# Optimization experiments

Measured on AMD Instinct MI355X. Metric: run time of the kernel, lower is better.

Reference implementation:

```python
import jax, jax.numpy as jnp
import numpy as np

B, D, C = 512, 16384, 3
SAMPLE_DURATION = 16
NEG_THRESHOLD = 0.5
NEGPOS_RATIO = 3


def setup_inputs() -> dict:
    key = jax.random.key(0)
    k1, k2, k3, k4, k5, k6, k7 = jax.random.split(key, 7)
    loc_pred = jax.random.normal(k1, (B, D, 2), dtype=jnp.float32)
    conf_pred = jax.random.normal(k2, (B, D, C), dtype=jnp.float32)
    # one ground-truth (start, end, label) per sample, within [0, 16]
    start = jax.random.uniform(k3, (B,), dtype=jnp.float32) * 8.0
    length = 1.0 + jax.random.uniform(k4, (B,), dtype=jnp.float32) * 7.0
    label = jax.random.randint(k5, (B,), 0, C).astype(jnp.float32)
    targets = jnp.stack([start, start + length, label], axis=-1)  # [B,3]
    # default bars stored as (center, length) in frame units
    centers = 1.0 + jax.random.uniform(k6, (D,), dtype=jnp.float32) * (SAMPLE_DURATION - 2.0)
    lengths = 1.0 + jax.random.uniform(k7, (D,), dtype=jnp.float32) * (SAMPLE_DURATION - 4.0)
    default_bar = jnp.stack([centers, lengths], axis=-1)  # [D,2]
    return {"loc_pred": loc_pred, "conf_pred": conf_pred,
            "targets": targets, "default_bar": default_bar}


def _match_one(truth, label, default):
    """truth [2]=(start,end), label scalar int, default [D,2]=(center,length).
    Returns loc_t [D,2], conf_t [D] (0=ignore, 1=background, >1=fg)."""
    d_c, d_l = default[:, 0], default[:, 1]
    d_s, d_e = d_c - d_l * 0.5, d_c + d_l * 0.5
    inter = jnp.clip(jnp.minimum(truth[1], d_e) - jnp.maximum(truth[0], d_s), 0.0)
    union = (truth[1] - truth[0]) + (d_e - d_s) - inter
    ov = inter / union                                   # [D] 1-D IoU
    best_prior = jnp.argmax(ov)                          # best anchor for the truth
    bto = ov.at[best_prior].set(2.0)                     # index_fill_ with 2
    conf = jnp.full((D,), label + 1, dtype=jnp.int32)    # single truth -> broadcast
    is_bg = conf == 1
    conf = jnp.where(bto < NEG_THRESHOLD, 0, conf)
    conf = jnp.where(is_bg, 1, conf)
    # SSD-style encoding of matched (start,end) against (center,length)
    m_c = (truth[0] + truth[1]) * 0.5
    m_l = truth[1] - truth[0]
    loc = jnp.stack([(m_c - d_c) / d_l, jnp.log(m_l / d_l)], axis=-1)  # [D,2]
    return loc, conf


def reference(loc_pred, conf_pred, targets, default_bar):
    truths = targets[:, :2]                              # [B,2]
    labels = targets[:, 2].astype(jnp.int32)             # [B]
    loc_t, conf_t = jax.vmap(_match_one, in_axes=(0, 0, None))(truths, labels, default_bar)
    loc_t = jax.lax.stop_gradient(loc_t)                 # built under no_grad in torch
    conf_t = jax.lax.stop_gradient(conf_t)

    pos = conf_t > 0                                     # [B,D] used for mining
    loc_pos = conf_t > 1                                 # [B,D] used for loc loss

    # SmoothL1 (beta=1), reduction='sum' over positives
    diff = loc_pred - loc_t
    ad = jnp.abs(diff)
    sl1 = jnp.where(ad < 1.0, 0.5 * diff * diff, ad - 0.5)
    loss_loc = jnp.sum(sl1 * loc_pos[..., None].astype(sl1.dtype))

    # hard-negative mining on per-anchor CE surrogate
    conf_tc = jnp.clip(conf_t - 1, 0)                    # [B,D] class ids 0..C-1
    lse = jax.nn.logsumexp(conf_pred, axis=-1)           # [B,D]
    gathered = jnp.take_along_axis(conf_pred, conf_tc[..., None], axis=-1)[..., 0]
    lc = lse - gathered
    lc = jnp.where(pos, 0.0, lc)
    loss_idx = jnp.argsort(-lc, axis=1)                  # descending sort
    idx_rank = jnp.argsort(loss_idx, axis=1)
    num_pos = jnp.sum(pos.astype(jnp.int32), axis=1, keepdims=True)   # [B,1]
    num_neg = jnp.clip(NEGPOS_RATIO * num_pos, max=D - 1)
    neg = idx_rank < num_neg                             # [B,D]

    sel = (pos | neg).astype(conf_pred.dtype)
    logp = jax.nn.log_softmax(conf_pred, axis=-1)
    ce = -jnp.take_along_axis(logp, conf_tc[..., None], axis=-1)[..., 0]
    loss_conf = jnp.sum(ce * sel)

    N = jnp.sum(num_pos).astype(loss_loc.dtype)
    return jnp.stack([loss_loc / N, loss_conf / N])
```

## Files before the change

kernel.cpp:

```cpp
#include <hip/hip_runtime.h>
#include <hip/hip_fp16.h>
#include <math.h>

constexpr int Bn = 512;
constexpr int Dn = 16384;
constexpr int BS = 512;
constexpr int CHUNKS = 16;
constexpr int CPRI = Dn / CHUNKS;
constexpr int K1T = 512;

__device__ __forceinline__ float lse3(float a, float b, float c) {
  float m = fmaxf(a, fmaxf(b, c));
  return m + __logf(__expf(a - m) + __expf(b - m) + __expf(c - m));
}
__device__ __forceinline__ float sl1f(float x) {
  float a = fabsf(x);
  return a < 1.f ? 0.5f * x * x : a - 0.5f;
}

__device__ __forceinline__ double blockReduceAddD(double v, double* sred) {
  int t = threadIdx.x;
  sred[t] = v;
  __syncthreads();
  for (int off = BS >> 1; off > 0; off >>= 1) {
    if (t < off) sred[t] += sred[t + off];
    __syncthreads();
  }
  double r = sred[0];
  __syncthreads();
  return r;
}

__global__ __launch_bounds__(K1T) void multiloss_stream(
    const float* __restrict__ loc_pred, const float* __restrict__ conf_pred,
    const float* __restrict__ targets, const float* __restrict__ default_bar,
    unsigned short* __restrict__ lc16,
    float* __restrict__ pce, float* __restrict__ plloc, int* __restrict__ pnpos)
{
  __shared__ float s_conf[CPRI * 3];
  __shared__ float s_bar[CPRI * 2];
  __shared__ unsigned short s_plist[CPRI];
  __shared__ float s_red[24];

  const int bid = blockIdx.x;
  const int b = bid >> 4, c = bid & 15;
  const int t = threadIdx.x;
  const int l = t & 63, w = t >> 6;
  const int wb = t & ~63;

  {
    const float4* srcC = (const float4*)(conf_pred + (size_t)b * Dn * 3) + (size_t)c * 768;
    float4* dstC = (float4*)s_conf;
    __builtin_amdgcn_global_load_lds(
        (const __attribute__((address_space(1))) void*)(srcC + t),
        (__attribute__((address_space(3))) void*)(dstC + wb), 16, 0, 0);
    if (t < 256)
      __builtin_amdgcn_global_load_lds(
          (const __attribute__((address_space(1))) void*)(srcC + 512 + t),
          (__attribute__((address_space(3))) void*)(dstC + 512 + wb), 16, 0, 0);
    const float4* srcB = (const float4*)default_bar + (size_t)c * 512;
    float4* dstB = (float4*)s_bar;
    __builtin_amdgcn_global_load_lds(
        (const __attribute__((address_space(1))) void*)(srcB + t),
        (__attribute__((address_space(3))) void*)(dstB + wb), 16, 0, 0);
  }

  const float t0  = targets[b * 3 + 0];
  const float t1  = targets[b * 3 + 1];
  const int   lab = (int)targets[b * 3 + 2];

  float ce = 0.f, lloc = 0.f; int npos = 0;
  const float m_c = (t0 + t1) * 0.5f;
  const float m_l = t1 - t0;
  const float T   = t1 - t0;

  __syncthreads();

  if (lab == 0) {
    #pragma unroll
    for (int i = 0; i < CPRI / K1T; ++i) {
      int p = i * K1T + t;
      float c0 = s_conf[3 * p], c1 = s_conf[3 * p + 1], c2 = s_conf[3 * p + 2];
      float hi = fmaxf(c0, c1), lo = fminf(c0, c1);
      float m  = fmaxf(hi, c2), mid = fminf(hi, c2);
      float s  = 1.f + __expf(lo - m) + __expf(mid - m);
      ce += (m - c0) + __logf(s);
    }
  } else {
    unsigned short* __restrict__ lcrow = lc16 + (size_t)b * Dn + (size_t)c * CPRI;
    unsigned wcnt = 0;
    unsigned short* plist = s_plist + (w << 7);
    #pragma unroll
    for (int i = 0; i < 2; ++i) {
      const int p = (w << 7) + (i << 6) + l;
      float c0 = s_conf[3 * p], c1 = s_conf[3 * p + 1], c2 = s_conf[3 * p + 2];
      float2 db = ((const float2*)s_bar)[p];
      float d_c = db.x, d_l = db.y;
      float d_s = __fmaf_rn(-0.5f, d_l, d_c);
      float d_e = __fmaf_rn(0.5f, d_l, d_c);
      float inter = fmaxf(fminf(t1, d_e) - fmaxf(t0, d_s), 0.f);
      float uni = (T + d_l) - inter;
      bool pos = (2.f * inter >= uni);
      npos += pos;
      float hi = fmaxf(c0, c1), lo = fminf(c0, c1);
      float m  = fmaxf(hi, c2), mid = fminf(hi, c2);
      float s  = 1.f + __expf(lo - m) + __expf(mid - m);
      float lnS = __logf(s);
      float cl = (lab == 1) ? c1 : c2;
      ce += pos ? ((m - cl) + lnS) : 0.f;
      float lcv = pos ? 0.f : ((m - c0) + lnS);
      lcrow[p] = __half_as_ushort(__float2half(lcv));
      unsigned long long mask = __ballot(pos);
      if (pos) {
        unsigned off = __builtin_amdgcn_mbcnt_hi((unsigned)(mask >> 32),
                       __builtin_amdgcn_mbcnt_lo((unsigned)mask, 0u));
        plist[wcnt + off] = (unsigned short)p;
      }
      wcnt += (unsigned)__popcll(mask);
    }
    const float log_ml = __logf(m_l);
    const float2* __restrict__ lp2 = (const float2*)loc_pred + (size_t)b * Dn + (size_t)c * CPRI;
    for (unsigned j = l; j < wcnt; j += 64) {
      int p = plist[j];
      float2 db = ((const float2*)s_bar)[p];
      float2 lp = lp2[p];
      float pd0 = lp.x - __fdividef(m_c - db.x, db.y);
      float pd1 = (lp.y - log_ml) + __logf(db.y);
      lloc += sl1f(pd0) + sl1f(pd1);
    }
  }

  #pragma unroll
  for (int off = 1; off < 64; off <<= 1) {
    ce   += __shfl_xor(ce, off);
    lloc += __shfl_xor(lloc, off);
    npos += __shfl_xor(npos, off);
  }
  if (l == 0) {
    s_red[w * 3 + 0] = ce; s_red[w * 3 + 1] = lloc; s_red[w * 3 + 2] = __int_as_float(npos);
  }
  __syncthreads();
  if (t == 0) {
    float Ce = 0.f, Ll = 0.f; int Np = 0;
    #pragma unroll
    for (int k = 0; k < 8; ++k) {
      Ce += s_red[k * 3 + 0]; Ll += s_red[k * 3 + 1]; Np += __float_as_int(s_red[k * 3 + 2]);
    }
    int pidx = b * CHUNKS + c;
    pce[pidx] = Ce; plloc[pidx] = Ll; pnpos[pidx] = Np;
  }
}

__global__ __launch_bounds__(BS) void multiloss_select(
    const float* __restrict__ loc_pred, const float* __restrict__ conf_pred,
    const float* __restrict__ targets, const float* __restrict__ default_bar,
    const unsigned short* __restrict__ lc16,
    const float* __restrict__ pce, const float* __restrict__ plloc,
    const int* __restrict__ pnpos,
    double* __restrict__ rloc, double* __restrict__ rconf, double* __restrict__ rnp)
{
  __shared__ unsigned short s_lc[Dn];
  __shared__ int      s_hist[256];
  __shared__ double   s_dred[BS];
  __shared__ float    s_fv[BS];
  __shared__ int      s_fi[BS];
  __shared__ unsigned s_wt[8];
  __shared__ unsigned s_sel[2];
  __shared__ double   s_sc[2];
  __shared__ int      s_np;

  const int b = blockIdx.x;
  const int t = threadIdx.x;
  const int lab = (int)targets[b * 3 + 2];

  if (lab == 0) {
    if (t == 0) {
      double ce = 0.0;
      for (int kk = 0; kk < CHUNKS; ++kk) ce += (double)pce[CHUNKS * b + kk];
      rloc[b] = 0.0; rconf[b] = ce; rnp[b] = (double)Dn;
    }
    return;
  }

  const float t0 = targets[b * 3 + 0];
  const float t1 = targets[b * 3 + 1];

  const float4* lcr = (const float4*)(lc16 + (size_t)b * Dn);
  float4* sl4 = (float4*)s_lc;
  #pragma unroll
  for (int j = 0; j < Dn / 8 / BS; ++j) sl4[j * BS + t] = lcr[j * BS + t];
  __syncthreads();

  if (t == 0) {
    double ce = 0.0, ll = 0.0; int np = 0;
    for (int kk = 0; kk < CHUNKS; ++kk) {
      int pi = CHUNKS * b + kk;
      ce += (double)pce[pi]; ll += (double)plloc[pi]; np += pnpos[pi];
    }
    s_sc[0] = ce; s_sc[1] = ll; s_np = np;
  }
  __syncthreads();
  int np = s_np;

  if (np == 0) {
    float bV = -1.f; int bI = 0;
    for (int d = t; d < Dn; d += BS) {
      float2 db = ((const float2*)default_bar)[d];
      float d_s = db.x - db.y * 0.5f;
      float d_e = db.x + db.y * 0.5f;
      float inter = fmaxf(fminf(t1, d_e) - fmaxf(t0, d_s), 0.f);
      float uni = (t1 - t0) + (d_e - d_s) - inter;
      float ov = inter / uni;
      if (ov > bV) { bV = ov; bI = d; }
    }
    s_fv[t] = bV; s_fi[t] = bI;
    __syncthreads();
    for (int off = BS >> 1; off > 0; off >>= 1) {
      if (t < off) {
        float v2 = s_fv[t + off]; int i2 = s_fi[t + off];
        if (v2 > s_fv[t] || (v2 == s_fv[t] && i2 < s_fi[t])) { s_fv[t] = v2; s_fi[t] = i2; }
      }
      __syncthreads();
    }
    if (t == 0) {
      int d = s_fi[0];
      const float* cp = conf_pred + (size_t)b * Dn * 3 + (size_t)d * 3;
      float c0 = cp[0], c1 = cp[1], c2 = cp[2];
      float lse = lse3(c0, c1, c2);
      float cl = (lab == 1) ? c1 : c2;
      float2 db = ((const float2*)default_bar)[d];
      float2 lp = ((const float2*)loc_pred)[(size_t)b * Dn + d];
      float m_c = (t0 + t1) * 0.5f, m_l = t1 - t0;
      float pd0 = lp.x - (m_c - db.x) / db.y;
      float pd1 = lp.y - __logf(m_l / db.y);
      s_sc[0] += (double)(lse - cl);
      s_sc[1] += (double)(sl1f(pd0) + sl1f(pd1));
      s_np = 1;
      s_lc[d] = 0;
    }
    __syncthreads();
    np = s_np;
  }
  const int k = min(3 * np, Dn - 1);

  unsigned prefix = 0;
  int K = k;
  const int lane = t & 63, w = t >> 6;
  for (int r = 0; r < 2; ++r) {
    if (t < 256) s_hist[t] = 0;
    __syncthreads();
    for (int d = t; d < Dn; d += BS) {
      unsigned u = s_lc[d];
      bool ok = (r == 0) || ((u >> 8) == prefix);
      if (ok) {
        unsigned bin = (r == 0) ? (u >> 8) : (u & 0xFFu);
        atomicAdd(&s_hist[bin], 1);
      }
    }
    __syncthreads();
    unsigned psum = (t < 256) ? (unsigned)s_hist[t] : 0u;
    unsigned incl = psum;
    #pragma unroll
    for (int off = 1; off < 64; off <<= 1) {
      unsigned v = __shfl_down(incl, off, 64);
      if (lane + off < 64) incl += v;
    }
    if (lane == 0) s_wt[w] = incl;
    __syncthreads();
    unsigned aboveW = 0;
    for (int w2 = w + 1; w2 < 8; ++w2) aboveW += s_wt[w2];
    const unsigned above = aboveW + (incl - psum);
    if (t < 256 && above < (unsigned)K && (unsigned)K <= above + psum) {
      s_sel[0] = (unsigned)t;
      s_sel[1] = above;
    }
    __syncthreads();
    unsigned selBin = s_sel[0];
    K -= (int)s_sel[1];
    prefix = (r == 0) ? selBin : ((prefix << 8) | selBin);
    __syncthreads();
  }
  const unsigned tb = prefix;

  float    ssum = 0.f;
  unsigned scnt = 0;
  for (int d = t; d < Dn; d += BS) {
    unsigned u = s_lc[d];
    if (u > tb) {
      ssum += __half2float(__ushort_as_half((unsigned short)u));
      scnt++;
    }
  }
  double S = blockReduceAddD((double)ssum, s_dred);
  double C = blockReduceAddD((double)scnt, s_dred);

  if (t == 0) {
    double tval = (double)__half2float(__ushort_as_half((unsigned short)tb));
    double topk = S + ((double)k - C) * tval;
    rloc[b]  = s_sc[1];
    rconf[b] = s_sc[0] + topk;
    rnp[b]   = (double)np;
  }
}

__global__ __launch_bounds__(BS) void multiloss_mono(
    const float* __restrict__ loc_pred, const float* __restrict__ conf_pred,
    const float* __restrict__ targets, const float* __restrict__ default_bar,
    double* __restrict__ rloc, double* __restrict__ rconf, double* __restrict__ rnp)
{
  __shared__ float    s_lc[Dn];
  __shared__ int      s_hist[2048];
  __shared__ unsigned s_scan[BS];
  __shared__ double   s_dred[BS];
  __shared__ unsigned s_sel[2];
  __shared__ double   s_corr[2];
  __shared__ int      s_np;

  const int b = blockIdx.x;
  const int t = threadIdx.x;

  const float t0  = targets[b * 3 + 0];
  const float t1  = targets[b * 3 + 1];
  const int   lab = (int)targets[b * 3 + 2];

  const float* __restrict__ cpb = conf_pred + (size_t)b * Dn * 3;

  if (lab == 0) {
    float ce = 0.f;
    for (int d = t; d < Dn; d += BS) {
      const float* cp = cpb + d * 3;
      ce += lse3(cp[0], cp[1], cp[2]) - cp[0];
    }
    double tot = blockReduceAddD((double)ce, s_dred);
    if (t == 0) { rloc[b] = 0.0; rconf[b] = tot; rnp[b] = (double)Dn; }
    return;
  }

  const float m_c = (t0 + t1) * 0.5f;
  const float m_l = t1 - t0;

  float bestV = -1.f; int bestI = 0;
  int   nposL = 0;
  float cePosL = 0.f;
  float llocL  = 0.f;

  for (int d = t; d < Dn; d += BS) {
    float2 db = ((const float2*)default_bar)[d];
    float d_c = db.x, d_l = db.y;
    float d_s = d_c - d_l * 0.5f;
    float d_e = d_c + d_l * 0.5f;
    float inter = fmaxf(fminf(t1, d_e) - fmaxf(t0, d_s), 0.f);
    float uni = (t1 - t0) + (d_e - d_s) - inter;
    float ov  = inter / uni;

    const float* cp = cpb + d * 3;
    float c0 = cp[0];
    float lse = lse3(cp[0], cp[1], cp[2]);

    if (ov > bestV) { bestV = ov; bestI = d; }

    float lcv;
    if (ov >= 0.5f) {
      nposL++;
      float cl = (lab == 1) ? cp[1] : cp[2];
      cePosL += lse - cl;
      float2 lp = ((const float2*)loc_pred)[(size_t)b * Dn + d];
      float pd0 = lp.x - (m_c - d_c) / d_l;
      float pd1 = lp.y - __logf(m_l / d_l);
      llocL += sl1f(pd0) + sl1f(pd1);
      lcv = 0.f;
    } else {
      lcv = lse - c0;
    }
    s_lc[d] = lcv;
  }

  float* sv = (float*)s_hist;
  int*   si = (int*)(s_hist + BS);
  sv[t] = bestV; si[t] = bestI;
  __syncthreads();
  for (int off = BS >> 1; off > 0; off >>= 1) {
    if (t < off) {
      float v2 = sv[t + off]; int i2 = si[t + off];
      if (v2 > sv[t] || (v2 == sv[t] && i2 < si[t])) { sv[t] = v2; si[t] = i2; }
    }
    __syncthreads();
  }
  float bV = sv[0]; int bI = si[0];
  __syncthreads();

  double nposTot  = blockReduceAddD((double)nposL, s_dred);
  double cePosTot = blockReduceAddD((double)cePosL, s_dred);
  double llocTot  = blockReduceAddD((double)llocL, s_dred);
  int num_pos = (int)(nposTot + 0.5);

  if (t == 0) {
    double cc = 0.0, lcor = 0.0; int np2 = num_pos;
    if (bV < 0.5f) {
      int d = bI;
      const float* cp = cpb + d * 3;
      float lse = lse3(cp[0], cp[1], cp[2]);
      float cl = (lab == 1) ? cp[1] : cp[2];
      cc = (double)(lse - cl);
      float2 db = ((const float2*)default_bar)[d];
      float2 lp = ((const float2*)loc_pred)[(size_t)b * Dn + d];
      float pd0 = lp.x - (m_c - db.x) / db.y;
      float pd1 = lp.y - __logf(m_l / db.y);
      lcor = (double)(sl1f(pd0) + sl1f(pd1));
      np2 += 1;
      s_lc[d] = 0.f;
    }
    s_corr[0] = cc; s_corr[1] = lcor; s_np = np2;
  }
  __syncthreads();
  int np = s_np;
  int k  = min(3 * np, Dn - 1);

  unsigned prefix = 0;
  int K = k;
  for (int r = 0; r < 3; ++r) {
    for (int i = t; i < 2048; i += BS) s_hist[i] = 0;
    __syncthreads();
    for (int d = t; d < Dn; d += BS) {
      unsigned u = __float_as_uint(s_lc[d]);
      bool ok = (r == 0) || (r == 1 ? ((u >> 21) == prefix) : ((u >> 10) == prefix));
      if (ok) {
        unsigned bin = (r == 0) ? (u >> 21)
                     : (r == 1) ? ((u >> 10) & 0x7FFu)
                                : (u & 0x3FFu);
        atomicAdd(&s_hist[bin], 1);
      }
    }
    __syncthreads();
    int nb  = (r == 2) ? 1024 : 2048;
    int per = nb / BS;
    unsigned psum = 0;
    for (int j = 0; j < per; ++j) psum += (unsigned)s_hist[t * per + j];
    s_scan[t] = psum;
    __syncthreads();
    for (int off = 1; off < BS; off <<= 1) {
      unsigned v = (t + off < BS) ? s_scan[t + off] : 0u;
      __syncthreads();
      s_scan[t] += v;
      __syncthreads();
    }
    unsigned above = (t < BS - 1) ? s_scan[t + 1] : 0u;
    if (above < (unsigned)K && (unsigned)K <= above + psum) {
      unsigned cum = above;
      int found = 0;
      for (int j = per - 1; j >= 0; --j) {
        unsigned c = (unsigned)s_hist[t * per + j];
        if (cum + c >= (unsigned)K) { found = j; break; }
        cum += c;
      }
      s_sel[0] = (unsigned)(t * per + found);
      s_sel[1] = cum;
    }
    __syncthreads();
    unsigned selBin = s_sel[0];
    K -= (int)s_sel[1];
    prefix = (r == 0) ? selBin
           : (r == 1) ? ((prefix << 11) | selBin)
                      : ((prefix << 10) | selBin);
    __syncthreads();
  }
  const unsigned tb = prefix;

  float    ssum = 0.f;
  unsigned scnt = 0;
  for (int d = t; d < Dn; d += BS) {
    float v = s_lc[d];
    if (__float_as_uint(v) > tb) { ssum += v; scnt++; }
  }
  double S = blockReduceAddD((double)ssum, s_dred);
  double C = blockReduceAddD((double)scnt, s_dred);

  if (t == 0) {
    double tval = (double)__uint_as_float(tb);
    double topk = S + ((double)k - C) * tval;
    rloc[b]  = llocTot + s_corr[1];
    rconf[b] = cePosTot + s_corr[0] + topk;
    rnp[b]   = (double)s_np;
  }
}

__global__ __launch_bounds__(512) void multiloss_final(
    const double* __restrict__ rloc, const double* __restrict__ rconf,
    const double* __restrict__ rnp, float* __restrict__ out)
{
  __shared__ double s1[512], s2[512], s3[512];
  int t = threadIdx.x;
  s1[t] = rloc[t];
  s2[t] = rconf[t];
  s3[t] = rnp[t];
  __syncthreads();
  for (int off = 256; off > 0; off >>= 1) {
    if (t < off) { s1[t] += s1[t + off]; s2[t] += s2[t + off]; s3[t] += s3[t + off]; }
    __syncthreads();
  }
  if (t == 0) {
    double N = s3[0];
    out[0] = (float)(s1[0] / N);
    out[1] = (float)(s2[0] / N);
  }
}

extern "C" void kernel_launch(void* const* d_in, const int* in_sizes, int n_in,
                              void* d_out, int out_size, void* d_ws, size_t ws_size,
                              hipStream_t stream) {
  const float* loc_pred    = (const float*)d_in[0];
  const float* conf_pred   = (const float*)d_in[1];
  const float* targets     = (const float*)d_in[2];
  const float* default_bar = (const float*)d_in[3];
  float* out = (float*)d_out;
  char* ws = (char*)d_ws;

  constexpr size_t LC_BYTES = (size_t)Bn * Dn * sizeof(unsigned short);
  constexpr size_t P_CNT = (size_t)Bn * CHUNKS;
  size_t off = LC_BYTES;
  float*  pce   = (float*)(ws + off); off += P_CNT * 4;
  float*  plloc = (float*)(ws + off); off += P_CNT * 4;
  int*    pnpos = (int*)(ws + off);   off += P_CNT * 4;
  double* rloc  = (double*)(ws + off); off += Bn * 8;
  double* rconf = (double*)(ws + off); off += Bn * 8;
  double* rnp   = (double*)(ws + off); off += Bn * 8;
  const size_t NEED = off;

  if (ws_size >= NEED) {
    hipLaunchKernelGGL(multiloss_stream, dim3(Bn * CHUNKS), dim3(K1T), 0, stream,
                       loc_pred, conf_pred, targets, default_bar,
                       (unsigned short*)ws, pce, plloc, pnpos);
    hipLaunchKernelGGL(multiloss_select, dim3(Bn), dim3(BS), 0, stream,
                       loc_pred, conf_pred, targets, default_bar,
                       (const unsigned short*)ws, pce, plloc, pnpos,
                       rloc, rconf, rnp);
    hipLaunchKernelGGL(multiloss_final, dim3(1), dim3(512), 0, stream,
                       rloc, rconf, rnp, out);
  } else {
    double* mloc  = (double*)ws;
    double* mconf = mloc + Bn;
    double* mnp   = mconf + Bn;
    hipLaunchKernelGGL(multiloss_mono, dim3(Bn), dim3(BS), 0, stream,
                       loc_pred, conf_pred, targets, default_bar, mloc, mconf, mnp);
    hipLaunchKernelGGL(multiloss_final, dim3(1), dim3(512), 0, stream,
                       mloc, mconf, mnp, out);
  }
}
```

Measured before the change: 62.05 us.

## Map two adjacent priors per thread with vector LDS reads and packed half2 stores

The streaming kernel now uses 32 chunks per batch row and 256-thread blocks. Each thread processes two adjacent priors, reading confidences and bars from LDS as float2/float4 vectors. It writes both surrogate losses as a single packed half2 word. The per-wave ballot/prefix compaction of positive priors is replaced by a direct predicated loc_pred load inside each lane. The aim is fewer LDS and global store instructions, no compaction overhead and more blocks in flight, at the cost of divergent, uncoalesced loc_pred loads for positives.

```diff
diff --git a/kernel.cpp b/kernel.cpp
--- a/kernel.cpp
+++ b/kernel.cpp
@@ -5,9 +5,9 @@
 constexpr int Bn = 512;
 constexpr int Dn = 16384;
 constexpr int BS = 512;
-constexpr int CHUNKS = 16;
+constexpr int CHUNKS = 32;
 constexpr int CPRI = Dn / CHUNKS;
-constexpr int K1T = 512;
+constexpr int K1T = 256;
 
 __device__ __forceinline__ float lse3(float a, float b, float c) {
   float m = fmaxf(a, fmaxf(b, c));
@@ -34,31 +34,30 @@
 __global__ __launch_bounds__(K1T) void multiloss_stream(
     const float* __restrict__ loc_pred, const float* __restrict__ conf_pred,
     const float* __restrict__ targets, const float* __restrict__ default_bar,
-    unsigned short* __restrict__ lc16,
+    unsigned* __restrict__ lc32,
     float* __restrict__ pce, float* __restrict__ plloc, int* __restrict__ pnpos)
 {
   __shared__ float s_conf[CPRI * 3];
   __shared__ float s_bar[CPRI * 2];
-  __shared__ unsigned short s_plist[CPRI];
-  __shared__ float s_red[24];
+  __shared__ float s_red[12];
 
   const int bid = blockIdx.x;
-  const int b = bid >> 4, c = bid & 15;
+  const int b = bid >> 5, c = bid & 31;
   const int t = threadIdx.x;
   const int l = t & 63, w = t >> 6;
   const int wb = t & ~63;
 
   {
-    const float4* srcC = (const float4*)(conf_pred + (size_t)b * Dn * 3) + (size_t)c * 768;
+    const float4* srcC = (const float4*)(conf_pred + (size_t)b * Dn * 3) + (size_t)c * (CPRI * 3 / 4);
     float4* dstC = (float4*)s_conf;
     __builtin_amdgcn_global_load_lds(
         (const __attribute__((address_space(1))) void*)(srcC + t),
         (__attribute__((address_space(3))) void*)(dstC + wb), 16, 0, 0);
-    if (t < 256)
+    if (t < 128)
       __builtin_amdgcn_global_load_lds(
-          (const __attribute__((address_space(1))) void*)(srcC + 512 + t),
-          (__attribute__((address_space(3))) void*)(dstC + 512 + wb), 16, 0, 0);
-    const float4* srcB = (const float4*)default_bar + (size_t)c * 512;
+          (const __attribute__((address_space(1))) void*)(srcC + 256 + t),
+          (__attribute__((address_space(3))) void*)(dstC + 256 + wb), 16, 0, 0);
+    const float4* srcB = (const float4*)default_bar + (size_t)c * (CPRI * 2 / 4);
     float4* dstB = (float4*)s_bar;
     __builtin_amdgcn_global_load_lds(
         (const __attribute__((address_space(1))) void*)(srcB + t),
@@ -71,63 +70,81 @@
 
   float ce = 0.f, lloc = 0.f; int npos = 0;
   const float m_c = (t0 + t1) * 0.5f;
-  const float m_l = t1 - t0;
   const float T   = t1 - t0;
 
   __syncthreads();
 
+  const float2 ca  = ((const float2*)s_conf)[3 * t];
+  const float2 cb  = ((const float2*)s_conf)[3 * t + 1];
+  const float2 cc_ = ((const float2*)s_conf)[3 * t + 2];
+
   if (lab == 0) {
-    #pragma unroll
-    for (int i = 0; i < CPRI / K1T; ++i) {
-      int p = i * K1T + t;
-      float c0 = s_conf[3 * p], c1 = s_conf[3 * p + 1], c2 = s_conf[3 * p + 2];
-      float hi = fmaxf(c0, c1), lo = fminf(c0, c1);
-      float m  = fmaxf(hi, c2), mid = fminf(hi, c2);
+    {
+      float hi = fmaxf(ca.x, ca.y), lo = fminf(ca.x, ca.y);
+      float m  = fmaxf(hi, cb.x),  mid = fminf(hi, cb.x);
       float s  = 1.f + __expf(lo - m) + __expf(mid - m);
-      ce += (m - c0) + __logf(s);
+      ce += (m - ca.x) + __logf(s);
+    }
+    {
+      float hi = fmaxf(cb.y, cc_.x), lo = fminf(cb.y, cc_.x);
+      float m  = fmaxf(hi, cc_.y),  mid = fminf(hi, cc_.y);
+      float s  = 1.f + __expf(lo - m) + __expf(mid - m);
+      ce += (m - cb.y) + __logf(s);
     }
   } else {
-    unsigned short* __restrict__ lcrow = lc16 + (size_t)b * Dn + (size_t)c * CPRI;
-    unsigned wcnt = 0;
-    unsigned short* plist = s_plist + (w << 7);
-    #pragma unroll
-    for (int i = 0; i < 2; ++i) {
-      const int p = (w << 7) + (i << 6) + l;
-      float c0 = s_conf[3 * p], c1 = s_conf[3 * p + 1], c2 = s_conf[3 * p + 2];
-      float2 db = ((const float2*)s_bar)[p];
-      float d_c = db.x, d_l = db.y;
-      float d_s = __fmaf_rn(-0.5f, d_l, d_c);
-      float d_e = __fmaf_rn(0.5f, d_l, d_c);
-      float inter = fmaxf(fminf(t1, d_e) - fmaxf(t0, d_s), 0.f);
-      float uni = (T + d_l) - inter;
+    const float log_ml = __logf(T);
+    const float2* __restrict__ lp2 = (const float2*)loc_pred + (size_t)b * Dn + (size_t)c * CPRI;
+    const float4 bb = ((const float4*)s_bar)[t];
+    float lcv0, lcv1;
+    const int pA = 2 * t;
+
+    {
+      float dc = bb.x, dl = bb.y;
+      float ds = __fmaf_rn(-0.5f, dl, dc);
+      float de = __fmaf_rn(0.5f, dl, dc);
+      float inter = fmaxf(fminf(t1, de) - fmaxf(t0, ds), 0.f);
+      float uni = (T + dl) - inter;
       bool pos = (2.f * inter >= uni);
-      npos += pos;
-      float hi = fmaxf(c0, c1), lo = fminf(c0, c1);
-      float m  = fmaxf(hi, c2), mid = fminf(hi, c2);
+      float hi = fmaxf(ca.x, ca.y), lo = fminf(ca.x, ca.y);
+      float m  = fmaxf(hi, cb.x),  mid = fminf(hi, cb.x);
       float s  = 1.f + __expf(lo - m) + __expf(mid - m);
       float lnS = __logf(s);
-      float cl = (lab == 1) ? c1 : c2;
+      float cl = (lab == 1) ? ca.y : cb.x;
+      npos += pos;
       ce += pos ? ((m - cl) + lnS) : 0.f;
-      float lcv = pos ? 0.f : ((m - c0) + lnS);
-      lcrow[p] = __half_as_ushort(__float2half(lcv));
-      unsigned long long mask = __ballot(pos);
+      lcv0 = pos ? 0.f : ((m - ca.x) + lnS);
       if (pos) {
-        unsigned off = __builtin_amdgcn_mbcnt_hi((unsigned)(mask >> 32),
-                       __builtin_amdgcn_mbcnt_lo((unsigned)mask, 0u));
-        plist[wcnt + off] = (unsigned short)p;
+        float2 lp = lp2[pA];
+        float pd0 = lp.x - __fdividef(m_c - dc, dl);
+        float pd1 = (lp.y - log_ml) + __logf(dl);
+        lloc += sl1f(pd0) + sl1f(pd1);
       }
-      wcnt += (unsigned)__popcll(mask);
-    }
-    const float log_ml = __logf(m_l);
-    const float2* __restrict__ lp2 = (const float2*)loc_pred + (size_t)b * Dn + (size_t)c * CPRI;
-    for (unsigned j = l; j < wcnt; j += 64) {
-      int p = plist[j];
-      float2 db = ((const float2*)s_bar)[p];
-      float2 lp = lp2[p];
-      float pd0 = lp.x - __fdividef(m_c - db.x, db.y);
-      float pd1 = (lp.y - log_ml) + __logf(db.y);
-      lloc += sl1f(pd0) + sl1f(pd1);
-    }
+    }
+    {
+      float dc = bb.z, dl = bb.w;
+      float ds = __fmaf_rn(-0.5f, dl, dc);
+      float de = __fmaf_rn(0.5f, dl, dc);
+      float inter = fmaxf(fminf(t1, de) - fmaxf(t0, ds), 0.f);
+      float uni = (T + dl) - inter;
+      bool pos = (2.f * inter >= uni);
+      float hi = fmaxf(cb.y, cc_.x), lo = fminf(cb.y, cc_.x);
+      float m  = fmaxf(hi, cc_.y),  mid = fminf(hi, cc_.y);
+      float s  = 1.f + __expf(lo - m) + __expf(mid - m);
+      float lnS = __logf(s);
+      float cl = (lab == 1) ? cc_.x : cc_.y;
+      npos += pos;
+      ce += pos ? ((m - cl) + lnS) : 0.f;
+      lcv1 = pos ? 0.f : ((m - cb.y) + lnS);
+      if (pos) {
+        float2 lp = lp2[pA + 1];
+        float pd0 = lp.x - __fdividef(m_c - dc, dl);
+        float pd1 = (lp.y - log_ml) + __logf(dl);
+        lloc += sl1f(pd0) + sl1f(pd1);
+      }
+    }
+    __half2 hv = __floats2half2_rn(lcv0, lcv1);
+    unsigned* lcrow = lc32 + ((size_t)b * Dn + (size_t)c * CPRI) / 2;
+    lcrow[t] = *reinterpret_cast<unsigned*>(&hv);
   }
 
   #pragma unroll
@@ -143,7 +160,7 @@
   if (t == 0) {
     float Ce = 0.f, Ll = 0.f; int Np = 0;
     #pragma unroll
-    for (int k = 0; k < 8; ++k) {
+    for (int k = 0; k < 4; ++k) {
       Ce += s_red[k * 3 + 0]; Ll += s_red[k * 3 + 1]; Np += __float_as_int(s_red[k * 3 + 2]);
     }
     int pidx = b * CHUNKS + c;
@@ -529,7 +546,7 @@
   if (ws_size >= NEED) {
     hipLaunchKernelGGL(multiloss_stream, dim3(Bn * CHUNKS), dim3(K1T), 0, stream,
                        loc_pred, conf_pred, targets, default_bar,
-                       (unsigned short*)ws, pce, plloc, pnpos);
+                       (unsigned*)ws, pce, plloc, pnpos);
     hipLaunchKernelGGL(multiloss_select, dim3(Bn), dim3(BS), 0, stream,
                        loc_pred, conf_pred, targets, default_bar,
                        (const unsigned short*)ws, pce, plloc, pnpos,
```

New measurement: 60.79 us. 2.0% less time.
